# Performance work log

Hardware: AMD Instinct MI355X
Metric: run time of the kernel (lower is better)

## Reference

```python
import jax, jax.numpy as jnp
import numpy as np

B, D, S = 8192, 1024, 32  # batch, feature dim, number of sessions (experts)


def setup_inputs() -> dict:
    key = jax.random.key(0)
    k1, k2, k3, k4 = jax.random.split(key, 4)
    x = jax.random.normal(k1, (B, D), dtype=jnp.float32)
    # Expert bank: original init is identity affine; perturb so the test is nontrivial.
    W = jnp.eye(D, dtype=jnp.float32)[None, :, :] + 0.02 * jax.random.normal(k2, (S, D, D), dtype=jnp.float32)
    b = 0.02 * jax.random.normal(k3, (S, D), dtype=jnp.float32)
    session_idx = jax.random.randint(k4, (B,), 0, S)  # int session id per sample
    return {"x": x, "W": W, "b": b, "session_idx": session_idx}


def reference(x, W, b, session_idx):
    """Per-sample session-affine dispatch: out[i] = W[session_idx[i]] @ x[i] + b[session_idx[i]].

    Implemented as a scan over the (small, fixed) set of S experts: one dense
    [B,D]x[D,D] GEMM per expert, masked-accumulated into the output. This avoids
    gathering a [B,D,D] per-sample weight tensor.
    """
    num_sessions = W.shape[0]

    def step(acc, packed):
        Ws, bs, s = packed                       # Ws: [D,D], bs: [D]
        y = x @ Ws.T + bs                        # [B,D] dense affine for expert s
        mask = (session_idx == s)[:, None]       # [B,1] samples belonging to s
        return acc + jnp.where(mask, y, jnp.zeros((), x.dtype)), None

    out, _ = jax.lax.scan(step, jnp.zeros_like(x), (W, b, jnp.arange(num_sessions)))
    return out
```

## Files before the change

### kernel.cpp

```cpp
#include <hip/hip_runtime.h>
#include <cstddef>

#define B_ROWS 8192
#define DIM    1024
#define NSESS  32
#define MT     128
#define NTILE  256
#define BK     64
#define KITERS (DIM / BK)
#define TPE    3
#define LROW   72
#define TSZA   (MT * LROW)
#define TSZB   (NTILE * LROW)
#define NXCD   8
#define EPX    (NSESS / NXCD)
#define BPE    (TPE * (DIM / NTILE))

typedef __attribute__((ext_vector_type(8))) short short8;
typedef __attribute__((ext_vector_type(4))) float floatx4;
typedef __attribute__((ext_vector_type(4))) int intx4;
typedef __attribute__((ext_vector_type(2))) unsigned int uintx2;

__device__ __forceinline__ unsigned pack_bf16_2(float fa, float fb) {
  unsigned a = __builtin_bit_cast(unsigned, fa);
  unsigned b = __builtin_bit_cast(unsigned, fb);
  a += 0x7fffu + ((a >> 16) & 1u);
  b += 0x7fffu + ((b >> 16) & 1u);
  return __builtin_amdgcn_perm(b, a, 0x07060302u);
}

__global__ __launch_bounds__(512, 2) void gemm_kernel(
    const float* __restrict__ x, const float* __restrict__ W,
    const float* __restrict__ bias, const int* __restrict__ sidx,
    float* __restrict__ out)
{
  __shared__ __align__(16) short As0[TSZA], As1[TSZA];
  __shared__ __align__(16) short Bs0[TSZB], Bs1[TSZB];
  __shared__ int row_ids[MT];
  __shared__ int psum[512];

  const int hw    = blockIdx.x;
  const int xcd   = hw & (NXCD - 1);
  const int r     = hw >> 3;
  const int s     = xcd * EPX + (r / BPE);
  const int rr    = r % BPE;
  const int ntile = rr / TPE;
  const int mtile = rr % TPE;
  const int tid   = threadIdx.x;

  const int lane = tid & 63;
  const int wv   = tid >> 6;
  const int wm   = wv >> 2;
  const int wn   = wv & 3;
  const int fr   = lane & 15;
  const int kg   = lane >> 4;

  const int srw = tid >> 4;
  const int sch = tid & 15;

  unsigned boff[8];
  floatx4 wr0[8], wr1[8];
  {
    const unsigned wbyte =
        (unsigned)(((size_t)s * DIM * DIM + (size_t)(ntile * NTILE) * DIM) * 4u);
#pragma unroll
    for (int j = 0; j < 8; ++j) {
      const int tr = j * 32 + srw;
      boff[j] = wbyte + (unsigned)((tr * DIM + sch * 4) * 4);
      wr0[j] = *(const floatx4*)((const char*)W + boff[j]);
    }
#pragma unroll
    for (int j = 0; j < 8; ++j)
      wr1[j] = *(const floatx4*)((const char*)W + boff[j] + (BK * 4));
  }

  const intx4* sv = (const intx4*)(sidx + tid * 16);
  int c = 0;
#pragma unroll
  for (int j = 0; j < 4; ++j) {
    const intx4 v = sv[j];
#pragma unroll
    for (int e = 0; e < 4; ++e) c += (v[e] == s);
  }
  psum[tid] = c;
  __syncthreads();
#pragma unroll
  for (int d = 1; d < 512; d <<= 1) {
    const int mine = psum[tid];
    const int add  = (tid >= d) ? psum[tid - d] : 0;
    __syncthreads();
    psum[tid] = mine + add;
    __syncthreads();
  }
  const int total = psum[511];
  const int nrows = (total - mtile * MT) < 0 ? 0
                  : ((total - mtile * MT) > MT ? MT : (total - mtile * MT));
  if (nrows == 0) return;
  const int base_rank = psum[tid] - c;

  if (tid < MT) row_ids[tid] = -1;
  __syncthreads();
  {
    int r2 = base_rank;
    const int lo = mtile * MT, hi = lo + MT;
#pragma unroll
    for (int j = 0; j < 4; ++j) {
      const intx4 v = sv[j];
#pragma unroll
      for (int e = 0; e < 4; ++e) {
        if (v[e] == s) {
          if (r2 >= lo && r2 < hi) row_ids[r2 - lo] = tid * 16 + 4 * j + e;
          ++r2;
        }
      }
    }
  }
  __syncthreads();

  unsigned aoff[4];
  floatx4 xr0[4], xr1[4];
#pragma unroll
  for (int j = 0; j < 4; ++j) {
    int ar = row_ids[j * 32 + srw];
    if (ar < 0) ar = 0;
    aoff[j] = (unsigned)((ar * DIM + sch * 4) * 4);
    xr0[j] = *(const floatx4*)((const char*)x + aoff[j]);
  }
#pragma unroll
  for (int j = 0; j < 4; ++j)
    xr1[j] = *(const floatx4*)((const char*)x + aoff[j] + (BK * 4));

  floatx4 acc[4][4] = {};

#define LOADSET(XR, WR, KB)                                                    \
  {                                                                            \
    _Pragma("unroll")                                                          \
    for (int j = 0; j < 4; ++j)                                                \
      XR[j] = *(const floatx4*)((const char*)x + aoff[j] + (KB) * (BK * 4));   \
    _Pragma("unroll")                                                          \
    for (int j = 0; j < 8; ++j)                                                \
      WR[j] = *(const floatx4*)((const char*)W + boff[j] + (KB) * (BK * 4));   \
  }

#define CVTWRITE(XR, WR, AS, BS)                                               \
  {                                                                            \
    _Pragma("unroll")                                                          \
    for (int j = 0; j < 4; ++j) {                                              \
      const int off = (j * 32 + srw) * LROW + sch * 4;                         \
      uintx2 ua = { pack_bf16_2(XR[j][0], XR[j][1]),                           \
                    pack_bf16_2(XR[j][2], XR[j][3]) };                         \
      *(uintx2*)&AS[off] = ua;                                                 \
    }                                                                          \
    _Pragma("unroll")                                                          \
    for (int j = 0; j < 8; ++j) {                                              \
      const int off = (j * 32 + srw) * LROW + sch * 4;                         \
      uintx2 ub = { pack_bf16_2(WR[j][0], WR[j][1]),                           \
                    pack_bf16_2(WR[j][2], WR[j][3]) };                         \
      *(uintx2*)&BS[off] = ub;                                                 \
    }                                                                          \
  }

#define COMPUTE(AS, BS)                                                        \
  {                                                                            \
    _Pragma("unroll")                                                          \
    for (int s2 = 0; s2 < 2; ++s2) {                                           \
      short8 fb[4];                                                            \
      _Pragma("unroll")                                                        \
      for (int i = 0; i < 4; ++i)                                              \
        fb[i] = *(const short8*)&BS[(wn * 64 + i * 16 + fr) * LROW + s2 * 32 + kg * 8]; \
      _Pragma("unroll")                                                        \
      for (int mi = 0; mi < 4; ++mi) {                                         \
        const short8 fa = *(const short8*)&AS[(wm * 64 + mi * 16 + fr) * LROW + s2 * 32 + kg * 8]; \
        _Pragma("unroll")                                                      \
        for (int ni = 0; ni < 4; ++ni)                                         \
          acc[mi][ni] = __builtin_amdgcn_mfma_f32_16x16x32_bf16(               \
              fa, fb[ni], acc[mi][ni], 0, 0, 0);                               \
      }                                                                        \
    }                                                                          \
  }

  CVTWRITE(xr0, wr0, As0, Bs0);
  __syncthreads();

  for (int kb = 0; kb < KITERS; kb += 2) {
    if (kb + 2 < KITERS) LOADSET(xr0, wr0, kb + 2);
    COMPUTE(As0, Bs0);
    CVTWRITE(xr1, wr1, As1, Bs1);
    __syncthreads();

    if (kb + 3 < KITERS) LOADSET(xr1, wr1, kb + 3);
    COMPUTE(As1, Bs1);
    if (kb + 2 < KITERS) {
      CVTWRITE(xr0, wr0, As0, Bs0);
    }
    __syncthreads();
  }

#undef LOADSET
#undef CVTWRITE
#undef COMPUTE

  __syncthreads();
  float* obuf = (float*)Bs0;
  const int col0 = ntile * NTILE + wn * 64;
  float bv[4];
#pragma unroll
  for (int ni = 0; ni < 4; ++ni) bv[ni] = bias[s * DIM + col0 + ni * 16 + fr];

  const int rbase = tid >> 6;
  const int ch    = tid & 63;

#pragma unroll
  for (int p = 0; p < 4; ++p) {
    if (wm == (p >> 1)) {
#pragma unroll
      for (int mh = 0; mh < 2; ++mh) {
        const int mi = (p & 1) * 2 + mh;
        const int lr = mi * 16 + kg * 4 - (p & 1) * 32;
#pragma unroll
        for (int q = 0; q < 4; ++q)
#pragma unroll
          for (int ni = 0; ni < 4; ++ni)
            obuf[(lr + q) * 260 + wn * 64 + ni * 16 + fr] = acc[mi][ni][q] + bv[ni];
      }
    }
    __syncthreads();
#pragma unroll
    for (int j = 0; j < 4; ++j) {
      const int lr = j * 8 + rbase;
      const int ml = p * 32 + lr;
      if (ml < nrows) {
        const int orow = row_ids[ml];
        const floatx4 v = *(const floatx4*)&obuf[lr * 260 + ch * 4];
        *(floatx4*)&out[(size_t)orow * DIM + ntile * NTILE + ch * 4] = v;
      }
    }
    __syncthreads();
  }
}

extern "C" void kernel_launch(void* const* d_in, const int* in_sizes, int n_in,
                              void* d_out, int out_size, void* d_ws, size_t ws_size,
                              hipStream_t stream) {
  const float* x    = (const float*)d_in[0];
  const float* W    = (const float*)d_in[1];
  const float* b    = (const float*)d_in[2];
  const int*   sidx = (const int*)d_in[3];
  float* out = (float*)d_out;
  (void)d_ws; (void)ws_size;

  hipLaunchKernelGGL(gemm_kernel, dim3(NSESS * TPE * (DIM / NTILE)), dim3(512),
                     0, stream, x, W, b, sidx, out);
}
```

Baseline: 275.1 us.

## Replace double-buffered LDS and two-deep register prefetch with single buffer

The GEMM main loop goes from two LDS buffers and two register prefetch sets to one LDS buffer and one register set, with an extra barrier before each LDS write. This halves LDS and prefetch-register use, which may ease occupancy pressure under the 512x2 launch bounds. In exchange, compute and the LDS writes of the next tile no longer overlap, and each k-step now has two barriers.

Result: slower. 316.2 us (+14.9%).

```diff
diff --git a/kernel.cpp b/kernel.cpp
--- a/kernel.cpp
+++ b/kernel.cpp
@@ -34,8 +34,7 @@
     const float* __restrict__ bias, const int* __restrict__ sidx,
     float* __restrict__ out)
 {
-  __shared__ __align__(16) short As0[TSZA], As1[TSZA];
-  __shared__ __align__(16) short Bs0[TSZB], Bs1[TSZB];
+  __shared__ __align__(16) short As[TSZA], Bs[TSZB];
   __shared__ int row_ids[MT];
   __shared__ int psum[512];
 
@@ -59,7 +58,7 @@
   const int sch = tid & 15;
 
   unsigned boff[8];
-  floatx4 wr0[8], wr1[8];
+  floatx4 wr[8];
   {
     const unsigned wbyte =
         (unsigned)(((size_t)s * DIM * DIM + (size_t)(ntile * NTILE) * DIM) * 4u);
@@ -67,11 +66,8 @@
     for (int j = 0; j < 8; ++j) {
       const int tr = j * 32 + srw;
       boff[j] = wbyte + (unsigned)((tr * DIM + sch * 4) * 4);
-      wr0[j] = *(const floatx4*)((const char*)W + boff[j]);
-    }
-#pragma unroll
-    for (int j = 0; j < 8; ++j)
-      wr1[j] = *(const floatx4*)((const char*)W + boff[j] + (BK * 4));
+      wr[j] = *(const floatx4*)((const char*)W + boff[j]);
+    }
   }
 
   const intx4* sv = (const intx4*)(sidx + tid * 16);
@@ -118,59 +114,56 @@
   __syncthreads();
 
   unsigned aoff[4];
-  floatx4 xr0[4], xr1[4];
+  floatx4 xr[4];
 #pragma unroll
   for (int j = 0; j < 4; ++j) {
     int ar = row_ids[j * 32 + srw];
     if (ar < 0) ar = 0;
     aoff[j] = (unsigned)((ar * DIM + sch * 4) * 4);
-    xr0[j] = *(const floatx4*)((const char*)x + aoff[j]);
-  }
-#pragma unroll
-  for (int j = 0; j < 4; ++j)
-    xr1[j] = *(const floatx4*)((const char*)x + aoff[j] + (BK * 4));
+    xr[j] = *(const floatx4*)((const char*)x + aoff[j]);
+  }
 
   floatx4 acc[4][4] = {};
 
-#define LOADSET(XR, WR, KB)                                                    \
+#define LOADREGS(KB)                                                           \
   {                                                                            \
     _Pragma("unroll")                                                          \
     for (int j = 0; j < 4; ++j)                                                \
-      XR[j] = *(const floatx4*)((const char*)x + aoff[j] + (KB) * (BK * 4));   \
+      xr[j] = *(const floatx4*)((const char*)x + aoff[j] + (KB) * (BK * 4));   \
     _Pragma("unroll")                                                          \
     for (int j = 0; j < 8; ++j)                                                \
-      WR[j] = *(const floatx4*)((const char*)W + boff[j] + (KB) * (BK * 4));   \
-  }
-
-#define CVTWRITE(XR, WR, AS, BS)                                               \
+      wr[j] = *(const floatx4*)((const char*)W + boff[j] + (KB) * (BK * 4));   \
+  }
+
+#define CVTWRITE()                                                             \
   {                                                                            \
     _Pragma("unroll")                                                          \
     for (int j = 0; j < 4; ++j) {                                              \
       const int off = (j * 32 + srw) * LROW + sch * 4;                         \
-      uintx2 ua = { pack_bf16_2(XR[j][0], XR[j][1]),                           \
-                    pack_bf16_2(XR[j][2], XR[j][3]) };                         \
-      *(uintx2*)&AS[off] = ua;                                                 \
+      uintx2 ua = { pack_bf16_2(xr[j][0], xr[j][1]),                           \
+                    pack_bf16_2(xr[j][2], xr[j][3]) };                         \
+      *(uintx2*)&As[off] = ua;                                                 \
     }                                                                          \
     _Pragma("unroll")                                                          \
     for (int j = 0; j < 8; ++j) {                                              \
       const int off = (j * 32 + srw) * LROW + sch * 4;                         \
-      uintx2 ub = { pack_bf16_2(WR[j][0], WR[j][1]),                           \
-                    pack_bf16_2(WR[j][2], WR[j][3]) };                         \
-      *(uintx2*)&BS[off] = ub;                                                 \
+      uintx2 ub = { pack_bf16_2(wr[j][0], wr[j][1]),                           \
+                    pack_bf16_2(wr[j][2], wr[j][3]) };                         \
+      *(uintx2*)&Bs[off] = ub;                                                 \
     }                                                                          \
   }
 
-#define COMPUTE(AS, BS)                                                        \
+#define COMPUTE()                                                              \
   {                                                                            \
     _Pragma("unroll")                                                          \
     for (int s2 = 0; s2 < 2; ++s2) {                                           \
       short8 fb[4];                                                            \
       _Pragma("unroll")                                                        \
       for (int i = 0; i < 4; ++i)                                              \
-        fb[i] = *(const short8*)&BS[(wn * 64 + i * 16 + fr) * LROW + s2 * 32 + kg * 8]; \
+        fb[i] = *(const short8*)&Bs[(wn * 64 + i * 16 + fr) * LROW + s2 * 32 + kg * 8]; \
       _Pragma("unroll")                                                        \
       for (int mi = 0; mi < 4; ++mi) {                                         \
-        const short8 fa = *(const short8*)&AS[(wm * 64 + mi * 16 + fr) * LROW + s2 * 32 + kg * 8]; \
+        const short8 fa = *(const short8*)&As[(wm * 64 + mi * 16 + fr) * LROW + s2 * 32 + kg * 8]; \
         _Pragma("unroll")                                                      \
         for (int ni = 0; ni < 4; ++ni)                                         \
           acc[mi][ni] = __builtin_amdgcn_mfma_f32_16x16x32_bf16(               \
@@ -179,29 +172,25 @@
     }                                                                          \
   }
 
-  CVTWRITE(xr0, wr0, As0, Bs0);
-  __syncthreads();
-
-  for (int kb = 0; kb < KITERS; kb += 2) {
-    if (kb + 2 < KITERS) LOADSET(xr0, wr0, kb + 2);
-    COMPUTE(As0, Bs0);
-    CVTWRITE(xr1, wr1, As1, Bs1);
-    __syncthreads();
-
-    if (kb + 3 < KITERS) LOADSET(xr1, wr1, kb + 3);
-    COMPUTE(As1, Bs1);
-    if (kb + 2 < KITERS) {
-      CVTWRITE(xr0, wr0, As0, Bs0);
-    }
-    __syncthreads();
-  }
-
-#undef LOADSET
+  CVTWRITE();
+  __syncthreads();
+
+  for (int kb = 0; kb < KITERS; ++kb) {
+    if (kb + 1 < KITERS) LOADREGS(kb + 1);
+    COMPUTE();
+    if (kb + 1 < KITERS) {
+      __syncthreads();
+      CVTWRITE();
+      __syncthreads();
+    }
+  }
+
+#undef LOADREGS
 #undef CVTWRITE
 #undef COMPUTE
 
   __syncthreads();
-  float* obuf = (float*)Bs0;
+  float* obuf = (float*)Bs;
   const int col0 = ntile * NTILE + wn * 64;
   float bv[4];
 #pragma unroll
```

## Enlarge M tile to 256 rows and halve K step to 32

Applied to the files above, without the earlier changes.

Raises the per-block row tile from 128 to 256, so each warp computes 8x4 MFMA fragments and fewer M tiles exist per expert (two instead of three). This gives more weight reuse per loaded W tile. The K step drops to 32, which shrinks LDS rows and keeps the double buffer in a single unified LDS array. In exchange it doubles the accumulator registers, which may hurt occupancy under launch_bounds(512,2), doubles the number of K iterations and barriers, and wastes more padded rows when an expert has fewer rows than the tile.

New measurement: 258.7 us. 6.0% less time.

```diff
diff --git a/kernel.cpp b/kernel.cpp
--- a/kernel.cpp
+++ b/kernel.cpp
@@ -4,14 +4,13 @@
 #define B_ROWS 8192
 #define DIM    1024
 #define NSESS  32
-#define MT     128
+#define MT     256
 #define NTILE  256
-#define BK     64
+#define BK     32
 #define KITERS (DIM / BK)
-#define TPE    3
-#define LROW   72
-#define TSZA   (MT * LROW)
-#define TSZB   (NTILE * LROW)
+#define TPE    2
+#define LROW   40
+#define TSZ    (MT * LROW)
 #define NXCD   8
 #define EPX    (NSESS / NXCD)
 #define BPE    (TPE * (DIM / NTILE))
@@ -34,18 +33,21 @@
     const float* __restrict__ bias, const int* __restrict__ sidx,
     float* __restrict__ out)
 {
-  __shared__ __align__(16) short As0[TSZA], As1[TSZA];
-  __shared__ __align__(16) short Bs0[TSZB], Bs1[TSZB];
+  __shared__ __align__(16) short lds[4 * TSZ];
   __shared__ int row_ids[MT];
   __shared__ int psum[512];
+  short* const As0 = lds;
+  short* const Bs0 = lds + TSZ;
+  short* const As1 = lds + 2 * TSZ;
+  short* const Bs1 = lds + 3 * TSZ;
 
   const int hw    = blockIdx.x;
   const int xcd   = hw & (NXCD - 1);
   const int r     = hw >> 3;
   const int s     = xcd * EPX + (r / BPE);
   const int rr    = r % BPE;
-  const int ntile = rr / TPE;
-  const int mtile = rr % TPE;
+  const int ntile = rr >> 1;
+  const int mtile = rr & 1;
   const int tid   = threadIdx.x;
 
   const int lane = tid & 63;
@@ -55,22 +57,22 @@
   const int fr   = lane & 15;
   const int kg   = lane >> 4;
 
-  const int srw = tid >> 4;
-  const int sch = tid & 15;
-
-  unsigned boff[8];
-  floatx4 wr0[8], wr1[8];
+  const int srw = tid >> 3;
+  const int sch = tid & 7;
+
+  unsigned boff[4];
+  floatx4 wr0[4], wr1[4];
   {
     const unsigned wbyte =
         (unsigned)(((size_t)s * DIM * DIM + (size_t)(ntile * NTILE) * DIM) * 4u);
 #pragma unroll
-    for (int j = 0; j < 8; ++j) {
-      const int tr = j * 32 + srw;
+    for (int j = 0; j < 4; ++j) {
+      const int tr = j * 64 + srw;
       boff[j] = wbyte + (unsigned)((tr * DIM + sch * 4) * 4);
       wr0[j] = *(const floatx4*)((const char*)W + boff[j]);
     }
 #pragma unroll
-    for (int j = 0; j < 8; ++j)
+    for (int j = 0; j < 4; ++j)
       wr1[j] = *(const floatx4*)((const char*)W + boff[j] + (BK * 4));
   }
 
@@ -121,7 +123,7 @@
   floatx4 xr0[4], xr1[4];
 #pragma unroll
   for (int j = 0; j < 4; ++j) {
-    int ar = row_ids[j * 32 + srw];
+    int ar = row_ids[j * 64 + srw];
     if (ar < 0) ar = 0;
     aoff[j] = (unsigned)((ar * DIM + sch * 4) * 4);
     xr0[j] = *(const floatx4*)((const char*)x + aoff[j]);
@@ -130,7 +132,7 @@
   for (int j = 0; j < 4; ++j)
     xr1[j] = *(const floatx4*)((const char*)x + aoff[j] + (BK * 4));
 
-  floatx4 acc[4][4] = {};
+  floatx4 acc[8][4] = {};
 
 #define LOADSET(XR, WR, KB)                                                    \
   {                                                                            \
@@ -138,7 +140,7 @@
     for (int j = 0; j < 4; ++j)                                                \
       XR[j] = *(const floatx4*)((const char*)x + aoff[j] + (KB) * (BK * 4));   \
     _Pragma("unroll")                                                          \
-    for (int j = 0; j < 8; ++j)                                                \
+    for (int j = 0; j < 4; ++j)                                                \
       WR[j] = *(const floatx4*)((const char*)W + boff[j] + (KB) * (BK * 4));   \
   }
 
@@ -146,36 +148,29 @@
   {                                                                            \
     _Pragma("unroll")                                                          \
     for (int j = 0; j < 4; ++j) {                                              \
-      const int off = (j * 32 + srw) * LROW + sch * 4;                         \
+      const int off = (j * 64 + srw) * LROW + sch * 4;                         \
       uintx2 ua = { pack_bf16_2(XR[j][0], XR[j][1]),                           \
                     pack_bf16_2(XR[j][2], XR[j][3]) };                         \
-      *(uintx2*)&AS[off] = ua;                                                 \
-    }                                                                          \
-    _Pragma("unroll")                                                          \
-    for (int j = 0; j < 8; ++j) {                                              \
-      const int off = (j * 32 + srw) * LROW + sch * 4;                         \
       uintx2 ub = { pack_bf16_2(WR[j][0], WR[j][1]),                           \
                     pack_bf16_2(WR[j][2], WR[j][3]) };                         \
+      *(uintx2*)&AS[off] = ua;                                                 \
       *(uintx2*)&BS[off] = ub;                                                 \
     }                                                                          \
   }
 
 #define COMPUTE(AS, BS)                                                        \
   {                                                                            \
-    _Pragma("unroll")                                                          \
-    for (int s2 = 0; s2 < 2; ++s2) {                                           \
-      short8 fb[4];                                                            \
+    short8 fb[4];                                                              \
+    _Pragma("unroll")                                                          \
+    for (int i = 0; i < 4; ++i)                                                \
+      fb[i] = *(const short8*)&BS[(wn * 64 + i * 16 + fr) * LROW + kg * 8];    \
+    _Pragma("unroll")                                                          \
+    for (int mi = 0; mi < 8; ++mi) {                                           \
+      const short8 fa = *(const short8*)&AS[(wm * 128 + mi * 16 + fr) * LROW + kg * 8]; \
       _Pragma("unroll")                                                        \
-      for (int i = 0; i < 4; ++i)                                              \
-        fb[i] = *(const short8*)&BS[(wn * 64 + i * 16 + fr) * LROW + s2 * 32 + kg * 8]; \
-      _Pragma("unroll")                                                        \
-      for (int mi = 0; mi < 4; ++mi) {                                         \
-        const short8 fa = *(const short8*)&AS[(wm * 64 + mi * 16 + fr) * LROW + s2 * 32 + kg * 8]; \
-        _Pragma("unroll")                                                      \
-        for (int ni = 0; ni < 4; ++ni)                                         \
-          acc[mi][ni] = __builtin_amdgcn_mfma_f32_16x16x32_bf16(               \
-              fa, fb[ni], acc[mi][ni], 0, 0, 0);                               \
-      }                                                                        \
+      for (int ni = 0; ni < 4; ++ni)                                           \
+        acc[mi][ni] = __builtin_amdgcn_mfma_f32_16x16x32_bf16(                 \
+            fa, fb[ni], acc[mi][ni], 0, 0, 0);                                 \
     }                                                                          \
   }
 
@@ -190,9 +185,7 @@
 
     if (kb + 3 < KITERS) LOADSET(xr1, wr1, kb + 3);
     COMPUTE(As1, Bs1);
-    if (kb + 2 < KITERS) {
-      CVTWRITE(xr0, wr0, As0, Bs0);
-    }
+    if (kb + 2 < KITERS) CVTWRITE(xr0, wr0, As0, Bs0);
     __syncthreads();
   }
 
@@ -201,7 +194,7 @@
 #undef COMPUTE
 
   __syncthreads();
-  float* obuf = (float*)Bs0;
+  float* obuf = (float*)lds;
   const int col0 = ntile * NTILE + wn * 64;
   float bv[4];
 #pragma unroll
@@ -211,12 +204,12 @@
   const int ch    = tid & 63;
 
 #pragma unroll
-  for (int p = 0; p < 4; ++p) {
-    if (wm == (p >> 1)) {
+  for (int p = 0; p < 8; ++p) {
+    if (wm == (p >> 2)) {
 #pragma unroll
       for (int mh = 0; mh < 2; ++mh) {
-        const int mi = (p & 1) * 2 + mh;
-        const int lr = mi * 16 + kg * 4 - (p & 1) * 32;
+        const int mi = (p & 3) * 2 + mh;
+        const int lr = mi * 16 + kg * 4 - (p & 3) * 32;
 #pragma unroll
         for (int q = 0; q < 4; ++q)
 #pragma unroll
```

## Use two balanced 192-row M tiles per expert with wave-shuffle scan

Applied to the files above, without the earlier changes.

Replaces three fixed 128-row M tiles per expert with two tiles of up to 192 rows that split each expert's rows evenly. This cuts the number of blocks and the weight tile reloads per expert, and stops tiles from being mostly empty. The 512-entry LDS prefix sum with many barriers becomes a warp shuffle scan plus a per-wave sum. Loads of x rows past nrows are skipped, and the epilogue stops early. The cost is more accumulator registers (6x4 MFMA tiles) and more LDS per block, which may lower occupancy under launch_bounds(512,2). If an expert has more than 384 rows, they no longer fit in two tiles.

Result: slower. 348.0 us (+26.5%).

```diff
diff --git a/kernel.cpp b/kernel.cpp
--- a/kernel.cpp
+++ b/kernel.cpp
@@ -4,11 +4,11 @@
 #define B_ROWS 8192
 #define DIM    1024
 #define NSESS  32
-#define MT     128
+#define MT     192
 #define NTILE  256
 #define BK     64
 #define KITERS (DIM / BK)
-#define TPE    3
+#define TPE    2
 #define LROW   72
 #define TSZA   (MT * LROW)
 #define TSZB   (NTILE * LROW)
@@ -34,18 +34,21 @@
     const float* __restrict__ bias, const int* __restrict__ sidx,
     float* __restrict__ out)
 {
-  __shared__ __align__(16) short As0[TSZA], As1[TSZA];
-  __shared__ __align__(16) short Bs0[TSZB], Bs1[TSZB];
+  __shared__ __align__(16) short lds[2 * (TSZA + TSZB)];
   __shared__ int row_ids[MT];
-  __shared__ int psum[512];
+  __shared__ int wsum[8];
+  short* const As0 = lds;
+  short* const Bs0 = lds + TSZA;
+  short* const As1 = lds + TSZA + TSZB;
+  short* const Bs1 = lds + 2 * TSZA + TSZB;
 
   const int hw    = blockIdx.x;
   const int xcd   = hw & (NXCD - 1);
   const int r     = hw >> 3;
   const int s     = xcd * EPX + (r / BPE);
   const int rr    = r % BPE;
-  const int ntile = rr / TPE;
-  const int mtile = rr % TPE;
+  const int ntile = rr >> 1;
+  const int mtile = rr & 1;
   const int tid   = threadIdx.x;
 
   const int lane = tid & 63;
@@ -82,27 +85,32 @@
 #pragma unroll
     for (int e = 0; e < 4; ++e) c += (v[e] == s);
   }
-  psum[tid] = c;
-  __syncthreads();
-#pragma unroll
-  for (int d = 1; d < 512; d <<= 1) {
-    const int mine = psum[tid];
-    const int add  = (tid >= d) ? psum[tid - d] : 0;
-    __syncthreads();
-    psum[tid] = mine + add;
-    __syncthreads();
-  }
-  const int total = psum[511];
-  const int nrows = (total - mtile * MT) < 0 ? 0
-                  : ((total - mtile * MT) > MT ? MT : (total - mtile * MT));
+  int ic = c;
+#pragma unroll
+  for (int d = 1; d < 64; d <<= 1) {
+    const int t = __shfl_up(ic, d);
+    if (lane >= d) ic += t;
+  }
+  if (lane == 63) wsum[wv] = ic;
+  __syncthreads();
+  int wbase = 0, total = 0;
+#pragma unroll
+  for (int w = 0; w < 8; ++w) {
+    const int v = wsum[w];
+    total += v;
+    if (w < wv) wbase += v;
+  }
+  const int h     = (total + 1) >> 1;
+  const int lo    = mtile * h;
+  const int hi    = mtile ? total : h;
+  const int nrows = hi - lo;
   if (nrows == 0) return;
-  const int base_rank = psum[tid] - c;
+  const int base_rank = wbase + ic - c;
 
   if (tid < MT) row_ids[tid] = -1;
   __syncthreads();
   {
     int r2 = base_rank;
-    const int lo = mtile * MT, hi = lo + MT;
 #pragma unroll
     for (int j = 0; j < 4; ++j) {
       const intx4 v = sv[j];
@@ -117,26 +125,29 @@
   }
   __syncthreads();
 
-  unsigned aoff[4];
-  floatx4 xr0[4], xr1[4];
-#pragma unroll
-  for (int j = 0; j < 4; ++j) {
+  unsigned aoff[6];
+  floatx4 xr0[6], xr1[6];
+#pragma unroll
+  for (int j = 0; j < 6; ++j) {
     int ar = row_ids[j * 32 + srw];
     if (ar < 0) ar = 0;
     aoff[j] = (unsigned)((ar * DIM + sch * 4) * 4);
-    xr0[j] = *(const floatx4*)((const char*)x + aoff[j]);
-  }
-#pragma unroll
-  for (int j = 0; j < 4; ++j)
-    xr1[j] = *(const floatx4*)((const char*)x + aoff[j] + (BK * 4));
-
-  floatx4 acc[4][4] = {};
+    if (j * 32 + srw < nrows)
+      xr0[j] = *(const floatx4*)((const char*)x + aoff[j]);
+  }
+#pragma unroll
+  for (int j = 0; j < 6; ++j)
+    if (j * 32 + srw < nrows)
+      xr1[j] = *(const floatx4*)((const char*)x + aoff[j] + (BK * 4));
+
+  floatx4 acc[6][4] = {};
 
 #define LOADSET(XR, WR, KB)                                                    \
   {                                                                            \
     _Pragma("unroll")                                                          \
-    for (int j = 0; j < 4; ++j)                                                \
-      XR[j] = *(const floatx4*)((const char*)x + aoff[j] + (KB) * (BK * 4));   \
+    for (int j = 0; j < 6; ++j)                                                \
+      if (j * 32 + srw < nrows)                                                \
+        XR[j] = *(const floatx4*)((const char*)x + aoff[j] + (KB) * (BK * 4)); \
     _Pragma("unroll")                                                          \
     for (int j = 0; j < 8; ++j)                                                \
       WR[j] = *(const floatx4*)((const char*)W + boff[j] + (KB) * (BK * 4));   \
@@ -145,7 +156,7 @@
 #define CVTWRITE(XR, WR, AS, BS)                                               \
   {                                                                            \
     _Pragma("unroll")                                                          \
-    for (int j = 0; j < 4; ++j) {                                              \
+    for (int j = 0; j < 6; ++j) {                                              \
       const int off = (j * 32 + srw) * LROW + sch * 4;                         \
       uintx2 ua = { pack_bf16_2(XR[j][0], XR[j][1]),                           \
                     pack_bf16_2(XR[j][2], XR[j][3]) };                         \
@@ -169,8 +180,8 @@
       for (int i = 0; i < 4; ++i)                                              \
         fb[i] = *(const short8*)&BS[(wn * 64 + i * 16 + fr) * LROW + s2 * 32 + kg * 8]; \
       _Pragma("unroll")                                                        \
-      for (int mi = 0; mi < 4; ++mi) {                                         \
-        const short8 fa = *(const short8*)&AS[(wm * 64 + mi * 16 + fr) * LROW + s2 * 32 + kg * 8]; \
+      for (int mi = 0; mi < 6; ++mi) {                                         \
+        const short8 fa = *(const short8*)&AS[(wm * 96 + mi * 16 + fr) * LROW + s2 * 32 + kg * 8]; \
         _Pragma("unroll")                                                      \
         for (int ni = 0; ni < 4; ++ni)                                         \
           acc[mi][ni] = __builtin_amdgcn_mfma_f32_16x16x32_bf16(               \
@@ -190,9 +201,7 @@
 
     if (kb + 3 < KITERS) LOADSET(xr1, wr1, kb + 3);
     COMPUTE(As1, Bs1);
-    if (kb + 2 < KITERS) {
-      CVTWRITE(xr0, wr0, As0, Bs0);
-    }
+    if (kb + 2 < KITERS) CVTWRITE(xr0, wr0, As0, Bs0);
     __syncthreads();
   }
 
@@ -200,8 +209,7 @@
 #undef CVTWRITE
 #undef COMPUTE
 
-  __syncthreads();
-  float* obuf = (float*)Bs0;
+  float* obuf = (float*)lds;
   const int col0 = ntile * NTILE + wn * 64;
   float bv[4];
 #pragma unroll
@@ -211,12 +219,13 @@
   const int ch    = tid & 63;
 
 #pragma unroll
-  for (int p = 0; p < 4; ++p) {
-    if (wm == (p >> 1)) {
+  for (int p = 0; p < 6; ++p) {
+    if (p * 32 >= nrows) break;
+    if (wm == (p >= 3 ? 1 : 0)) {
 #pragma unroll
       for (int mh = 0; mh < 2; ++mh) {
-        const int mi = (p & 1) * 2 + mh;
-        const int lr = mi * 16 + kg * 4 - (p & 1) * 32;
+        const int mi = (p % 3) * 2 + mh;
+        const int lr = mi * 16 + kg * 4 - (p % 3) * 32;
 #pragma unroll
         for (int q = 0; q < 4; ++q)
 #pragma unroll
```
